# Optimization experiments

Hardware: AMD Instinct MI355X
Metric: run time of the kernel (lower is better)

Reference implementation:

```python
import jax, jax.numpy as jnp
import numpy as np

B = 512      # graphs per batch
NPG = 62     # nodes (electrodes) per graph
N = B * NPG  # total nodes per band
F_IN = 5     # node features
H = 8        # attention heads
C = 3        # num_classes (GATConv out channels, concat=False)
DEG = 16     # avg degree
EG = NPG * DEG
E = B * EG   # edges per band
NB = 5       # bands: delta, alpha, beta, theta, gamma
DE_DIM = 930 # 310*3


def setup_inputs() -> dict:
    key = jax.random.key(0)
    ks = jax.random.split(key, 24)
    x_bands = jax.random.normal(ks[0], (NB, N, F_IN), dtype=jnp.float32)
    # within-graph random edges: node ids in [g*62, g*62+62)
    base = (jnp.arange(B, dtype=jnp.int32) * NPG)[None, :, None]
    src = jax.random.randint(ks[1], (NB, B, EG), 0, NPG, dtype=jnp.int32) + base
    dst = jax.random.randint(ks[2], (NB, B, EG), 0, NPG, dtype=jnp.int32) + base
    edge_index_bands = jnp.stack([src.reshape(NB, E), dst.reshape(NB, E)], axis=1)  # [NB,2,E]
    batch = jnp.repeat(jnp.arange(B, dtype=jnp.int32), NPG)  # [N]
    de = jax.random.normal(ks[3], (B, NPG, 5, 3), dtype=jnp.float32)
    s = 0.3
    params = dict(
        bn_gamma=jnp.ones((NB, F_IN), jnp.float32),
        bn_beta=jnp.zeros((NB, F_IN), jnp.float32),
        W=jax.random.normal(ks[4], (NB, F_IN, H * C)) * s,
        att_src=jax.random.normal(ks[5], (NB, H, C)) * s,
        att_dst=jax.random.normal(ks[6], (NB, H, C)) * s,
        gat_bias=jax.random.normal(ks[7], (NB, C)) * 0.01,
        fg_W=jax.random.normal(ks[8], (NB * C, 64)) * s,
        fg_b=jnp.zeros((64,), jnp.float32),
        ln_g=jnp.ones((DE_DIM,), jnp.float32),
        ln_b=jnp.zeros((DE_DIM,), jnp.float32),
        q_W=jax.random.normal(ks[9], (DE_DIM, 64)) * 0.03,
        q_b=jnp.zeros((64,), jnp.float32),
        k_W=jax.random.normal(ks[10], (DE_DIM, 64)) * 0.03,
        k_b=jnp.zeros((64,), jnp.float32),
        v_W=jax.random.normal(ks[11], (DE_DIM, 64)) * 0.03,
        v_b=jnp.zeros((64,), jnp.float32),
        fa_W=jax.random.normal(ks[12], (128, C)) * s,
        fa_b=jnp.zeros((C,), jnp.float32),
    )
    return dict(x_bands=x_bands, edge_index_bands=edge_index_bands, batch=batch, de=de, **params)


def _gat_band(x, ei, g, b, Wb, a_src, a_dst, bias, batch):
    # BatchNorm1d (training-mode batch stats), eps=1e-5
    mu = x.mean(0)
    var = x.var(0)
    xn = (x - mu) * jax.lax.rsqrt(var + 1e-5) * g + b
    # GATConv(F_IN -> C, heads=H, concat=False) with self-loops
    xt = (xn @ Wb).reshape(N, H, C)                       # [N,H,C]
    al_s = (xt * a_src).sum(-1)                           # [N,H]
    al_d = (xt * a_dst).sum(-1)                           # [N,H]
    loop = jnp.arange(N, dtype=ei.dtype)
    src = jnp.concatenate([ei[0], loop])                  # [E+N]
    dst = jnp.concatenate([ei[1], loop])
    e = jax.nn.leaky_relu(al_s[src] + al_d[dst], 0.2)     # [E+N,H]
    m = jax.ops.segment_max(e, dst, num_segments=N)
    ex = jnp.exp(e - m[dst])
    denom = jax.ops.segment_sum(ex, dst, num_segments=N)  # [N,H]
    msg = ex[:, :, None] * xt[src]                        # [E+N,H,C]
    out = jax.ops.segment_sum(msg, dst, num_segments=N) / denom[:, :, None]
    out = out.mean(1) + bias                              # concat=False -> head mean
    out = jax.nn.elu(out)
    # global_mean_pool
    summed = jax.ops.segment_sum(out, batch, num_segments=B)
    cnt = jax.ops.segment_sum(jnp.ones((N,), out.dtype), batch, num_segments=B)
    return summed / cnt[:, None]                          # [B,C]


def reference(x_bands, edge_index_bands, batch, de, bn_gamma, bn_beta, W,
              att_src, att_dst, gat_bias, fg_W, fg_b, ln_g, ln_b,
              q_W, q_b, k_W, k_b, v_W, v_b, fa_W, fa_b):
    pooled = jax.vmap(_gat_band, in_axes=(0, 0, 0, 0, 0, 0, 0, 0, None))(
        x_bands, edge_index_bands, bn_gamma, bn_beta, W, att_src, att_dst, gat_bias, batch
    )  # [NB,B,C]
    x_concat = jnp.transpose(pooled, (1, 0, 2)).reshape(B, NB * C)  # [B,15]
    x_out = jax.nn.elu(x_concat @ fg_W + fg_b)                       # [B,64]
    # de branch: LayerNorm + self-attention
    de_f = de.reshape(B, DE_DIM)
    mu = de_f.mean(-1, keepdims=True)
    var = de_f.var(-1, keepdims=True)
    de_n = (de_f - mu) * jax.lax.rsqrt(var + 1e-5) * ln_g + ln_b
    Q = de_n @ q_W + q_b
    K = de_n @ k_W + k_b
    V = de_n @ v_W + v_b
    attn = jax.nn.softmax(Q @ K.T / jnp.sqrt(jnp.float32(64)), axis=-1)
    x_de = attn @ V                                                  # [B,64]
    # F.leaky_relu(x, negative_slope=1) is the identity
    out = jnp.concatenate([x_out, x_de], axis=1) @ fa_W + fa_b       # [B,3]
    return jax.nn.elu(out)
```

## Files before the change

kernel.cpp:

```cpp
#include <hip/hip_runtime.h>
#include <math.h>

#define NBANDS 5
#define BATCH  512
#define NPG    62
#define NTOT   (BATCH*NPG)
#define F_IN   5
#define NH     8
#define NC     3
#define HC     (NH*NC)
#define EG     (NPG*16)
#define ETOT   (BATCH*EG)
#define EPG    (EG+NPG)
#define DE_DIM 930
#define KS     5
#define KLEN   186
#define XTS    9

#define WS_BN     0
#define WS_LNS    512
#define WS_POOLED 1536
#define WS_Q      (WS_POOLED + NBANDS*BATCH*NC)
#define WS_KT     (WS_Q  + BATCH*64)
#define WS_V      (WS_KT + BATCH*64)
#define WS_PART   (WS_V  + BATCH*64)
#define WS_END    (WS_PART + 3*KS*BATCH*64)

__device__ __forceinline__ float eluf(float x) { return x > 0.f ? x : expm1f(x); }

__global__ __launch_bounds__(256) void stats_kernel(
    const float* __restrict__ x, const float* __restrict__ de,
    float* __restrict__ ws) {
    int bid = blockIdx.x;
    int tid = threadIdx.x;
    int w = tid >> 6, lane = tid & 63;
    if (bid < 40) {
        int band = bid >> 3, chunk = bid & 7;
        const int G4 = NTOT / 8 / 4;
        const float4* xb4 =
            (const float4*)(x + (size_t)band * NTOT * F_IN) + (size_t)chunk * G4 * 5;
        float s[F_IN] = {0,0,0,0,0}, q[F_IN] = {0,0,0,0,0};
        for (int gi = tid; gi < G4; gi += 256) {
            const float4* p4 = xb4 + (size_t)gi * 5;
            float vv[20];
            *(float4*)&vv[0]  = p4[0];
            *(float4*)&vv[4]  = p4[1];
            *(float4*)&vv[8]  = p4[2];
            *(float4*)&vv[12] = p4[3];
            *(float4*)&vv[16] = p4[4];
            #pragma unroll
            for (int i = 0; i < 20; ++i) { float v = vv[i]; s[i % 5] += v; q[i % 5] += v * v; }
        }
        #pragma unroll
        for (int f = 0; f < F_IN; ++f) {
            for (int off = 32; off; off >>= 1) {
                s[f] += __shfl_down(s[f], off, 64);
                q[f] += __shfl_down(q[f], off, 64);
            }
        }
        __shared__ float part[4][10];
        if (lane == 0) {
            #pragma unroll
            for (int f = 0; f < F_IN; ++f) { part[w][f] = s[f]; part[w][5 + f] = q[f]; }
        }
        __syncthreads();
        if (tid < 10) {
            float t = part[0][tid] + part[1][tid] + part[2][tid] + part[3][tid];
            ws[WS_BN + (band * 8 + chunk) * 10 + tid] = t;
        }
    } else {
        int r = (bid - 40) * 4 + w;
        const float* row = de + (size_t)r * DE_DIM;
        float s1 = 0.f, s2 = 0.f;
        for (int i = lane; i < DE_DIM; i += 64) { float v = row[i]; s1 += v; s2 += v * v; }
        #pragma unroll
        for (int off = 32; off; off >>= 1) {
            s1 += __shfl_down(s1, off, 64);
            s2 += __shfl_down(s2, off, 64);
        }
        if (lane == 0) {
            float mu  = s1 * (1.0f / DE_DIM);
            float var = s2 * (1.0f / DE_DIM) - mu * mu;
            ws[WS_LNS + r * 2]     = mu;
            ws[WS_LNS + r * 2 + 1] = rsqrtf(var + 1e-5f);
        }
    }
}

__global__ __launch_bounds__(256) void gat_kernel(
    const float* __restrict__ x, const int* __restrict__ ei,
    const float* __restrict__ bn_g, const float* __restrict__ bn_b,
    const float* __restrict__ Wg, const float* __restrict__ attSg,
    const float* __restrict__ attDg, const float* __restrict__ biasg,
    const float* __restrict__ wsbn, float* __restrict__ pooled) {
    int g    = blockIdx.x;
    int band = blockIdx.y;
    __shared__ float  Wl[F_IN * HC];
    __shared__ float  attS[HC], attD[HC];
    __shared__ float  bnsum[10];
    __shared__ float  scale[F_IN], shift[F_IN];
    __shared__ float  xns[NPG * F_IN];
    __shared__ float4 xt4[NPG * XTS];
    __shared__ float  ald[NPG * NH];
    __shared__ int    deg[NPG];
    __shared__ int    offs[NPG + 1];
    __shared__ int    cur[NPG];
    __shared__ int    csr[EPG];
    __shared__ float  outd[NPG][NC];

    int tid = threadIdx.x;
    int lane = tid & 63;
    int nbase = g * NPG;

    if (tid < F_IN * HC) Wl[tid] = Wg[band * F_IN * HC + tid];
    if (tid >= 128 && tid < 128 + HC) attS[tid - 128] = attSg[band * HC + tid - 128];
    if (tid >= 160 && tid < 160 + HC) attD[tid - 160] = attDg[band * HC + tid - 160];
    if (tid < NPG) deg[tid] = 0;
    if (tid >= 192 && tid < 202) {
        int f = tid - 192;
        float t = 0.f;
        #pragma unroll
        for (int c = 0; c < 8; ++c) t += wsbn[(band * 8 + c) * 10 + f];
        bnsum[f] = t;
    }
    __syncthreads();

    const int* srcp = ei + (size_t)band * 2 * ETOT + (size_t)g * EG;
    const int* dstp = srcp + ETOT;

    for (int e = tid; e < EG; e += 256) atomicAdd(&deg[dstp[e] - nbase], 1);
    if (tid < F_IN) {
        float mu  = bnsum[tid] * (1.0f / NTOT);
        float var = bnsum[5 + tid] * (1.0f / NTOT) - mu * mu;
        float sc  = rsqrtf(var + 1e-5f) * bn_g[band * F_IN + tid];
        scale[tid] = sc;
        shift[tid] = bn_b[band * F_IN + tid] - mu * sc;
    }
    __syncthreads();

    {
        const float* xr = x + (size_t)band * NTOT * F_IN + (size_t)nbase * F_IN;
        for (int i = tid; i < NPG * F_IN; i += 256) {
            int f = i % F_IN;
            xns[i] = xr[i] * scale[f] + shift[f];
        }
    }
    if (tid >= 64 && tid < 128) {
        int l = lane;
        int dv = (l < NPG) ? deg[l] + 1 : 0;
        int sc = dv;
        #pragma unroll
        for (int off = 1; off < 64; off <<= 1) {
            int t = __shfl_up(sc, off, 64);
            if (l >= off) sc += t;
        }
        if (l < NPG) offs[l + 1] = sc;
        if (l == 0)  offs[0] = 0;
    }
    __syncthreads();

    for (int p = tid; p < NPG * NH; p += 256) {
        int n = p >> 3, h = p & 7;
        float c0 = 0.f, c1 = 0.f, c2 = 0.f;
        #pragma unroll
        for (int f = 0; f < F_IN; ++f) {
            float xv = xns[n * F_IN + f];
            c0 += xv * Wl[f * HC + h * NC + 0];
            c1 += xv * Wl[f * HC + h * NC + 1];
            c2 += xv * Wl[f * HC + h * NC + 2];
        }
        float as = c0 * attS[h * NC] + c1 * attS[h * NC + 1] + c2 * attS[h * NC + 2];
        float ad = c0 * attD[h * NC] + c1 * attD[h * NC + 1] + c2 * attD[h * NC + 2];
        xt4[n * XTS + h] = make_float4(c0, c1, c2, as);
        ald[p] = ad;
    }
    if (tid < NPG) { int o0 = offs[tid]; csr[o0] = tid; cur[tid] = o0 + 1; }
    __syncthreads();

    for (int e = tid; e < EG; e += 256) {
        int ld = dstp[e] - nbase;
        int p = atomicAdd(&cur[ld], 1);
        csr[p] = srcp[e] - nbase;
    }
    __syncthreads();

    for (int p = tid; p < NPG * NH; p += 256) {
        int d = p >> 3, h = p & 7;
        int s0 = offs[d], s1 = offs[d + 1];
        float adv = ald[p];
        float den = 0.f, m0 = 0.f, m1 = 0.f, m2 = 0.f;
        for (int e = s0; e < s1; ++e) {
            int s = csr[e];
            float4 t = xt4[s * XTS + h];
            float v = t.w + adv;
            v = v > 0.f ? v : 0.2f * v;
            float ex = __expf(v);
            den += ex;
            m0 += ex * t.x;
            m1 += ex * t.y;
            m2 += ex * t.z;
        }
        float rd = 1.0f / den;
        float o0 = m0 * rd, o1 = m1 * rd, o2 = m2 * rd;
        #pragma unroll
        for (int off = 1; off < 8; off <<= 1) {
            o0 += __shfl_xor(o0, off, 64);
            o1 += __shfl_xor(o1, off, 64);
            o2 += __shfl_xor(o2, off, 64);
        }
        if (h == 0) { outd[d][0] = o0; outd[d][1] = o1; outd[d][2] = o2; }
    }
    __syncthreads();

    float oc[NC] = {0.f, 0.f, 0.f};
    if (tid < NPG) {
        #pragma unroll
        for (int c = 0; c < NC; ++c)
            oc[c] = eluf(outd[tid][c] * (1.0f / NH) + biasg[band * NC + c]);
    }
    if (tid < 64) {
        #pragma unroll
        for (int c = 0; c < NC; ++c) {
            float v = oc[c];
            for (int off = 32; off; off >>= 1) v += __shfl_down(v, off, 64);
            if (tid == 0)
                pooled[((size_t)band * BATCH + g) * NC + c] = v * (1.0f / NPG);
        }
    }
}

__global__ __launch_bounds__(256) void qkv_partial(
    const float* __restrict__ de, const float* __restrict__ lns,
    const float* __restrict__ ln_g, const float* __restrict__ ln_b,
    const float* __restrict__ qW, const float* __restrict__ kW,
    const float* __restrict__ vW, float* __restrict__ part) {
    int rt = blockIdx.x;
    int m  = blockIdx.y;
    int ks = blockIdx.z;
    __shared__ float dl[4][KLEN];
    int tid = threadIdx.x, w = tid >> 6, col = tid & 63;
    for (int i = tid; i < 4 * KLEN; i += 256) {
        int rr = i / KLEN, ii = i - rr * KLEN;
        int row = rt * 4 + rr, gcol = ks * KLEN + ii;
        float mu = lns[row * 2], rstd = lns[row * 2 + 1];
        dl[rr][ii] = (de[(size_t)row * DE_DIM + gcol] - mu) * rstd * ln_g[gcol] + ln_b[gcol];
    }
    __syncthreads();
    const float* Wm = ((m == 0) ? qW : (m == 1) ? kW : vW) + (size_t)ks * KLEN * 64;
    float a[6] = {0, 0, 0, 0, 0, 0};
    for (int i = 0; i < KLEN; i += 6) {
        #pragma unroll
        for (int j = 0; j < 6; ++j)
            a[j] += dl[w][i + j] * Wm[(size_t)(i + j) * 64 + col];
    }
    float acc = ((a[0] + a[1]) + (a[2] + a[3])) + (a[4] + a[5]);
    part[(((size_t)m * KS + ks) * BATCH + rt * 4 + w) * 64 + col] = acc;
}

__global__ __launch_bounds__(256) void qkv_reduce(
    const float* __restrict__ part,
    const float* __restrict__ qb, const float* __restrict__ kb,
    const float* __restrict__ vb,
    float* __restrict__ Q, float* __restrict__ KT, float* __restrict__ V) {
    int idx = blockIdx.x * 256 + threadIdx.x;
    int m  = idx >> 15;
    int local = idx & 32767;
    if (m == 1) {
        int row = local & 511, col = local >> 9;
        float s = 0.f;
        #pragma unroll
        for (int ks = 0; ks < KS; ++ks)
            s += part[(((size_t)KS + ks) << 15) + (row << 6) + col];
        KT[local] = s + kb[col];
    } else {
        int col = local & 63;
        float s = 0.f;
        #pragma unroll
        for (int ks = 0; ks < KS; ++ks)
            s += part[(((size_t)m * KS + ks) << 15) + local];
        s += (m == 0) ? qb[col] : vb[col];
        ((m == 0) ? Q : V)[local] = s;
    }
}

__global__ __launch_bounds__(256) void qkv_fused_fb(
    const float* __restrict__ de, const float* __restrict__ ln_g,
    const float* __restrict__ ln_b,
    const float* __restrict__ qW, const float* __restrict__ qb,
    const float* __restrict__ kW, const float* __restrict__ kb,
    const float* __restrict__ vW, const float* __restrict__ vb,
    float* __restrict__ Q, float* __restrict__ KT, float* __restrict__ V) {
    int r0 = blockIdx.x * 4;
    int m  = blockIdx.y;
    __shared__ float dn[4][DE_DIM];
    int tid  = threadIdx.x;
    int w    = tid >> 6, lane = tid & 63;
    const float* row = de + (size_t)(r0 + w) * DE_DIM;
    float s1 = 0.f, s2 = 0.f;
    for (int i = lane; i < DE_DIM; i += 64) {
        float v = row[i]; dn[w][i] = v; s1 += v; s2 += v * v;
    }
    #pragma unroll
    for (int off = 32; off; off >>= 1) {
        s1 += __shfl_down(s1, off, 64);
        s2 += __shfl_down(s2, off, 64);
    }
    float mu   = __shfl(s1, 0, 64) * (1.0f / DE_DIM);
    float var  = __shfl(s2, 0, 64) * (1.0f / DE_DIM) - mu * mu;
    float rstd = rsqrtf(var + 1e-5f);
    for (int i = lane; i < DE_DIM; i += 64)
        dn[w][i] = (dn[w][i] - mu) * rstd * ln_g[i] + ln_b[i];
    __syncthreads();
    const float* Wm = (m == 0) ? qW : (m == 1) ? kW : vW;
    const float* bm = (m == 0) ? qb : (m == 1) ? kb : vb;
    float a[10];
    #pragma unroll
    for (int j = 0; j < 10; ++j) a[j] = 0.f;
    for (int i = 0; i < DE_DIM; i += 10) {
        #pragma unroll
        for (int j = 0; j < 10; ++j)
            a[j] += dn[w][i + j] * Wm[(size_t)(i + j) * 64 + lane];
    }
    float acc = (((a[0] + a[1]) + (a[2] + a[3])) + ((a[4] + a[5]) + (a[6] + a[7])))
              + (a[8] + a[9]) + bm[lane];
    int r = r0 + w;
    if (m == 1) KT[lane * BATCH + r] = acc;
    else ((m == 0) ? Q : V)[(size_t)r * 64 + lane] = acc;
}

__global__ __launch_bounds__(256) void attn_final(
    const float* __restrict__ Q, const float* __restrict__ KT,
    const float* __restrict__ V, const float* __restrict__ pooled,
    const float* __restrict__ fgW, const float* __restrict__ fgb,
    const float* __restrict__ faW, const float* __restrict__ fab,
    float* __restrict__ out) {
    int b = blockIdx.x;
    int tid = threadIdx.x;
    __shared__ float qrow[64];
    __shared__ float p[BATCH];
    __shared__ float red[8];
    __shared__ float pv[4][64];
    __shared__ float xde[64], xout[64];
    if (tid < 64) qrow[tid] = Q[(size_t)b * 64 + tid];
    __syncthreads();

    float a0 = 0.f, a1 = 0.f, b0 = 0.f, b1 = 0.f;
    #pragma unroll 8
    for (int i = 0; i < 64; i += 2) {
        float q0 = qrow[i], q1 = qrow[i + 1];
        a0 += q0 * KT[(size_t)i * BATCH + tid];
        a1 += q1 * KT[(size_t)(i + 1) * BATCH + tid];
        b0 += q0 * KT[(size_t)i * BATCH + tid + 256];
        b1 += q1 * KT[(size_t)(i + 1) * BATCH + tid + 256];
    }
    float sj0 = (a0 + a1) * 0.125f, sj1 = (b0 + b1) * 0.125f;

    float mx = fmaxf(sj0, sj1);
    for (int off = 32; off; off >>= 1) mx = fmaxf(mx, __shfl_down(mx, off, 64));
    if ((tid & 63) == 0) red[tid >> 6] = mx;
    __syncthreads();
    mx = fmaxf(fmaxf(red[0], red[1]), fmaxf(red[2], red[3]));
    float e0 = __expf(sj0 - mx), e1 = __expf(sj1 - mx);
    p[tid] = e0; p[tid + 256] = e1;
    float s = e0 + e1;
    for (int off = 32; off; off >>= 1) s += __shfl_down(s, off, 64);
    if ((tid & 63) == 0) red[4 + (tid >> 6)] = s;
    __syncthreads();
    float denom = red[4] + red[5] + red[6] + red[7];

    int o = tid & 63, cq = tid >> 6;
    float acc = 0.f;
    #pragma unroll 4
    for (int j = cq * 128; j < cq * 128 + 128; ++j)
        acc += p[j] * V[(size_t)j * 64 + o];
    pv[cq][o] = acc;
    __syncthreads();
    if (tid < 64)
        xde[tid] = (pv[0][tid] + pv[1][tid] + pv[2][tid] + pv[3][tid]) / denom;
    if (tid >= 64 && tid < 128) {
        int oo = tid - 64;
        float a = fgb[oo];
        #pragma unroll
        for (int j = 0; j < NBANDS * NC; ++j) {
            int band = j / NC, c = j % NC;
            a += pooled[((size_t)band * BATCH + b) * NC + c] * fgW[j * 64 + oo];
        }
        xout[oo] = eluf(a);
    }
    __syncthreads();
    if (tid < NC) {
        float a = fab[tid];
        for (int i = 0; i < 64; ++i) a += xout[i] * faW[i * NC + tid];
        for (int i = 0; i < 64; ++i) a += xde[i] * faW[(64 + i) * NC + tid];
        out[(size_t)b * NC + tid] = eluf(a);
    }
}

extern "C" void kernel_launch(void* const* d_in, const int* in_sizes, int n_in,
                              void* d_out, int out_size, void* d_ws, size_t ws_size,
                              hipStream_t stream) {
    const float* x     = (const float*)d_in[0];
    const int*   ei    = (const int*)  d_in[1];
    const float* de    = (const float*)d_in[3];
    const float* bn_g  = (const float*)d_in[4];
    const float* bn_b  = (const float*)d_in[5];
    const float* W     = (const float*)d_in[6];
    const float* attS  = (const float*)d_in[7];
    const float* attD  = (const float*)d_in[8];
    const float* gbias = (const float*)d_in[9];
    const float* fgW   = (const float*)d_in[10];
    const float* fgb   = (const float*)d_in[11];
    const float* ln_g  = (const float*)d_in[12];
    const float* ln_b  = (const float*)d_in[13];
    const float* qW    = (const float*)d_in[14];
    const float* qb    = (const float*)d_in[15];
    const float* kW    = (const float*)d_in[16];
    const float* kb    = (const float*)d_in[17];
    const float* vW    = (const float*)d_in[18];
    const float* vb    = (const float*)d_in[19];
    const float* faW   = (const float*)d_in[20];
    const float* fab   = (const float*)d_in[21];
    float* ws  = (float*)d_ws;
    float* out = (float*)d_out;

    stats_kernel<<<168, 256, 0, stream>>>(x, de, ws);
    gat_kernel<<<dim3(BATCH, NBANDS), 256, 0, stream>>>(
        x, ei, bn_g, bn_b, W, attS, attD, gbias, ws + WS_BN, ws + WS_POOLED);

    if (ws_size >= (size_t)WS_END * sizeof(float)) {
        qkv_partial<<<dim3(BATCH / 4, 3, KS), 256, 0, stream>>>(
            de, ws + WS_LNS, ln_g, ln_b, qW, kW, vW, ws + WS_PART);
        qkv_reduce<<<(3 * BATCH * 64) / 256, 256, 0, stream>>>(
            ws + WS_PART, qb, kb, vb, ws + WS_Q, ws + WS_KT, ws + WS_V);
    } else {
        qkv_fused_fb<<<dim3(BATCH / 4, 3), 256, 0, stream>>>(
            de, ln_g, ln_b, qW, qb, kW, kb, vW, vb,
            ws + WS_Q, ws + WS_KT, ws + WS_V);
    }
    attn_final<<<BATCH, 256, 0, stream>>>(ws + WS_Q, ws + WS_KT, ws + WS_V,
                                          ws + WS_POOLED, fgW, fgb, faW, fab, out);
}
```

Measured before the change: 69.73 us.

## Load-balance GAT edge aggregation with flat per-thread edge chunks and shared atomics

Replaces the per-(node,head) edge loop with a flat partition of all (head, edge) items into equal chunks per thread. Each thread binary-searches its starting node, accumulates segment partials and flushes them to shared memory with atomicAdd. The aim is to remove load imbalance from varying in-degree, since the old version left half the threads idle on 496 work items. It also narrows CSR indices to 16-bit and moves BN scale computation earlier to drop a barrier. In exchange it adds an extra barrier, shared-memory float atomics and binary-search overhead per thread, and the race in the h==0 write-back into msgm that other lanes read needs care.

```diff
diff --git a/kernel.cpp b/kernel.cpp
--- a/kernel.cpp
+++ b/kernel.cpp
@@ -105,8 +105,8 @@
     __shared__ int    deg[NPG];
     __shared__ int    offs[NPG + 1];
     __shared__ int    cur[NPG];
-    __shared__ int    csr[EPG];
-    __shared__ float  outd[NPG][NC];
+    __shared__ unsigned short csr[EPG];
+    __shared__ float  msgm[NPG * NH * 4];
 
     int tid = threadIdx.x;
     int lane = tid & 63;
@@ -116,6 +116,7 @@
     if (tid >= 128 && tid < 128 + HC) attS[tid - 128] = attSg[band * HC + tid - 128];
     if (tid >= 160 && tid < 160 + HC) attD[tid - 160] = attDg[band * HC + tid - 160];
     if (tid < NPG) deg[tid] = 0;
+    for (int i = tid; i < NPG * NH * 4; i += 256) msgm[i] = 0.f;
     if (tid >= 192 && tid < 202) {
         int f = tid - 192;
         float t = 0.f;
@@ -123,21 +124,20 @@
         for (int c = 0; c < 8; ++c) t += wsbn[(band * 8 + c) * 10 + f];
         bnsum[f] = t;
     }
+    if (tid >= 192 && tid < 192 + F_IN) {
+        int f = tid - 192;
+        float mu  = bnsum[f] * (1.0f / NTOT);
+        float var = bnsum[5 + f] * (1.0f / NTOT) - mu * mu;
+        float sc  = rsqrtf(var + 1e-5f) * bn_g[band * F_IN + f];
+        scale[f] = sc;
+        shift[f] = bn_b[band * F_IN + f] - mu * sc;
+    }
     __syncthreads();
 
     const int* srcp = ei + (size_t)band * 2 * ETOT + (size_t)g * EG;
     const int* dstp = srcp + ETOT;
 
     for (int e = tid; e < EG; e += 256) atomicAdd(&deg[dstp[e] - nbase], 1);
-    if (tid < F_IN) {
-        float mu  = bnsum[tid] * (1.0f / NTOT);
-        float var = bnsum[5 + tid] * (1.0f / NTOT) - mu * mu;
-        float sc  = rsqrtf(var + 1e-5f) * bn_g[band * F_IN + tid];
-        scale[tid] = sc;
-        shift[tid] = bn_b[band * F_IN + tid] - mu * sc;
-    }
-    __syncthreads();
-
     {
         const float* xr = x + (size_t)band * NTOT * F_IN + (size_t)nbase * F_IN;
         for (int i = tid; i < NPG * F_IN; i += 256) {
@@ -145,6 +145,8 @@
             xns[i] = xr[i] * scale[f] + shift[f];
         }
     }
+    __syncthreads();
+
     if (tid >= 64 && tid < 128) {
         int l = lane;
         int dv = (l < NPG) ? deg[l] + 1 : 0;
@@ -157,8 +159,6 @@
         if (l < NPG) offs[l + 1] = sc;
         if (l == 0)  offs[0] = 0;
     }
-    __syncthreads();
-
     for (int p = tid; p < NPG * NH; p += 256) {
         int n = p >> 3, h = p & 7;
         float c0 = 0.f, c1 = 0.f, c2 = 0.f;
@@ -174,49 +174,85 @@
         xt4[n * XTS + h] = make_float4(c0, c1, c2, as);
         ald[p] = ad;
     }
-    if (tid < NPG) { int o0 = offs[tid]; csr[o0] = tid; cur[tid] = o0 + 1; }
+    __syncthreads();
+
+    if (tid < NPG) {
+        int o0 = offs[tid];
+        csr[o0] = (unsigned short)tid;
+        cur[tid] = o0 + 1;
+    }
     __syncthreads();
 
     for (int e = tid; e < EG; e += 256) {
         int ld = dstp[e] - nbase;
         int p = atomicAdd(&cur[ld], 1);
-        csr[p] = srcp[e] - nbase;
+        csr[p] = (unsigned short)(srcp[e] - nbase);
+    }
+    __syncthreads();
+
+    {
+        const int NITEM = EPG * NH;
+        const int CHUNK = (NITEM + 255) / 256;
+        int i0 = tid * CHUNK;
+        int i1 = i0 + CHUNK; if (i1 > NITEM) i1 = NITEM;
+        if (i0 < i1) {
+            int h = i0 / EPG;
+            int e = i0 - h * EPG;
+            int lo = 0, hi = NPG;
+            while (lo + 1 < hi) { int mid = (lo + hi) >> 1; if (offs[mid] <= e) lo = mid; else hi = mid; }
+            int d = lo;
+            int bnd = offs[d + 1];
+            float adv = ald[d * NH + h];
+            float a0 = 0.f, a1 = 0.f, a2 = 0.f, aw = 0.f;
+            for (int i = i0; i < i1; ++i) {
+                int s = csr[e];
+                float4 t = xt4[s * XTS + h];
+                float v = t.w + adv;
+                v = v > 0.f ? v : 0.2f * v;
+                float ex = __expf(v);
+                a0 += ex * t.x; a1 += ex * t.y; a2 += ex * t.z; aw += ex;
+                ++e;
+                bool segend = (e >= bnd);
+                if (segend || i + 1 == i1) {
+                    float* m = &msgm[(d * NH + h) * 4];
+                    atomicAdd(m + 0, a0); atomicAdd(m + 1, a1);
+                    atomicAdd(m + 2, a2); atomicAdd(m + 3, aw);
+                    a0 = a1 = a2 = aw = 0.f;
+                    if (segend) {
+                        ++d;
+                        if (e >= EPG) { e = 0; d = 0; ++h; }
+                        if (i + 1 < i1) { bnd = offs[d + 1]; adv = ald[d * NH + h]; }
+                    }
+                }
+            }
+        }
     }
     __syncthreads();
 
     for (int p = tid; p < NPG * NH; p += 256) {
         int d = p >> 3, h = p & 7;
-        int s0 = offs[d], s1 = offs[d + 1];
-        float adv = ald[p];
-        float den = 0.f, m0 = 0.f, m1 = 0.f, m2 = 0.f;
-        for (int e = s0; e < s1; ++e) {
-            int s = csr[e];
-            float4 t = xt4[s * XTS + h];
-            float v = t.w + adv;
-            v = v > 0.f ? v : 0.2f * v;
-            float ex = __expf(v);
-            den += ex;
-            m0 += ex * t.x;
-            m1 += ex * t.y;
-            m2 += ex * t.z;
-        }
-        float rd = 1.0f / den;
-        float o0 = m0 * rd, o1 = m1 * rd, o2 = m2 * rd;
+        const float* m = &msgm[p * 4];
+        float rd = 1.0f / m[3];
+        float o0 = m[0] * rd, o1 = m[1] * rd, o2 = m[2] * rd;
         #pragma unroll
         for (int off = 1; off < 8; off <<= 1) {
             o0 += __shfl_xor(o0, off, 64);
             o1 += __shfl_xor(o1, off, 64);
             o2 += __shfl_xor(o2, off, 64);
         }
-        if (h == 0) { outd[d][0] = o0; outd[d][1] = o1; outd[d][2] = o2; }
+        if (h == 0) {
+            float* od = &msgm[(d * NH) * 4];
+            od[0] = o0; od[1] = o1; od[2] = o2;
+        }
     }
     __syncthreads();
 
     float oc[NC] = {0.f, 0.f, 0.f};
     if (tid < NPG) {
+        const float* od = &msgm[(tid * NH) * 4];
         #pragma unroll
         for (int c = 0; c < NC; ++c)
-            oc[c] = eluf(outd[tid][c] * (1.0f / NH) + biasg[band * NC + c]);
+            oc[c] = eluf(od[c] * (1.0f / NH) + biasg[band * NC + c]);
     }
     if (tid < 64) {
         #pragma unroll
```

Result: slower. 106.5 us (+52.7%).
